# Optimization experiments

Measured on AMD Instinct MI355X. Metric: run time of the kernel, lower is better.

Reference implementation:

```python
import jax, jax.numpy as jnp
import numpy as np
from jax import lax

B, T, IN, H = 128, 1024, 130, 512


def setup_inputs() -> dict:
    key = jax.random.key(0)
    ks = jax.random.split(key, 6)
    inputs = jax.random.normal(ks[0], (B, T, IN), dtype=jnp.float32)
    # valid lengths in [1, T] (forward indexes outputs[len-1])
    inputs_len = jax.random.randint(ks[1], (B,), 1, T + 1)
    h0 = jnp.zeros((B, H), dtype=jnp.float32)
    c0 = jnp.zeros((B, H), dtype=jnp.float32)
    s = 1.0 / np.sqrt(H)
    W_ih = jax.random.uniform(ks[2], (4 * H, IN - 2), jnp.float32, -s, s)
    W_hh = jax.random.uniform(ks[3], (4 * H, H), jnp.float32, -s, s)
    b_ih = jax.random.uniform(ks[4], (4 * H,), jnp.float32, -s, s)
    b_hh = jax.random.uniform(ks[5], (4 * H,), jnp.float32, -s, s)
    return {"inputs": inputs, "inputs_len": inputs_len, "h0": h0, "c0": c0,
            "W_ih": W_ih, "W_hh": W_hh, "b_ih": b_ih, "b_hh": b_hh}


def _lstm_encode(inputs, h0, c0, W_ih, W_hh, b_ih, b_hh):
    # drop last 2 features (coordinates), as in stard_LSTM branch
    x = inputs[..., :-2]                                   # [B, T, IN-2]
    # precompute input projections for all timesteps (same math as per-step)
    xproj = jnp.einsum('bti,gi->tbg', x, W_ih) + b_ih + b_hh  # [T, B, 4H]

    def step(carry, xw):
        h, c = carry
        gates = xw + h @ W_hh.T                            # [B, 4H]
        i, f, g, o = jnp.split(gates, 4, axis=-1)
        i = jax.nn.sigmoid(i)
        f = jax.nn.sigmoid(f)
        g = jnp.tanh(g)
        o = jax.nn.sigmoid(o)
        c2 = f * c + i * g
        h2 = o * jnp.tanh(c2)
        return (h2, c2), h2

    _, hs = lax.scan(step, (h0, c0), xproj)                # hs: [T, B, H]
    return hs


def reference(inputs, inputs_len, h0, c0, W_ih, W_hh, b_ih, b_hh):
    hs = _lstm_encode(inputs, h0, c0, W_ih, W_hh, b_ih, b_hh)
    # gather hidden state at last valid timestep per sequence
    b_idx = jnp.arange(inputs.shape[0])
    return hs[inputs_len - 1, b_idx]                       # [B, H]
```

## Files before the change

### kernel.cpp

```cpp
#include <hip/hip_runtime.h>
#include <hip/hip_bf16.h>
#include <cstdint>
#include <cstddef>

#define T_STEPS 1024
#define BATCH   128
#define INF     128
#define HID     512
#define NBLK    256
#define NTHR    256
#define PK      648

typedef _Float16 f16x8 __attribute__((ext_vector_type(8)));
typedef float    f32x4 __attribute__((ext_vector_type(4)));

static __device__ __forceinline__ unsigned short f16b(float v) {
  _Float16 h = (_Float16)v;
  unsigned short u;
  __builtin_memcpy(&u, &h, 2);
  return u;
}
static __device__ __forceinline__ float fsigmoid(float x) {
  return 1.f / (1.f + __expf(-x));
}
static __device__ __forceinline__ float ftanh(float x) {
  return 1.f - 2.f / (__expf(2.f * x) + 1.f);
}


__global__ __launch_bounds__(256) void k_prep_x(const float* __restrict__ in,
                                                unsigned short* __restrict__ xp)
{
  int t = blockIdx.x >> 3, bg = blockIdx.x & 7;
  int tid = threadIdx.x;
  size_t base = (size_t)blockIdx.x * 2048;
  #pragma unroll
  for (int rep = 0; rep < 8; ++rep) {
    int idx = rep * 256 + tid;
    int c = idx >> 7, k = idx & 127;
    float v = in[((size_t)(bg * 16 + c) * T_STEPS + t) * 130 + k];
    xp[base + c * 128 + k] = f16b(v);
  }
}

__global__ __launch_bounds__(64) void k_prep_w(const float* __restrict__ Wih,
                                               const float* __restrict__ Whh,
                                               unsigned short* __restrict__ wf)
{
  int blk = blockIdx.x;
  int s = blk % 20; int r = blk / 20;
  int u4 = r & 3; int ug = r >> 2;
  int l = threadIdx.x;
  int m = l & 15;
  int Grow = (m & 3) * HID + ug * 16 + u4 * 4 + (m >> 2);
  int kb = s * 32 + (l >> 4) * 8;
  unsigned short o[8];
  #pragma unroll
  for (int j = 0; j < 8; ++j) {
    float v = (kb + j < INF) ? Wih[(size_t)Grow * INF + kb + j]
                             : Whh[(size_t)Grow * HID + (kb + j - INF)];
    o[j] = f16b(v);
  }
  unsigned short* d = wf + ((size_t)blk * 64 + l) * 8;
  #pragma unroll
  for (int j = 0; j < 8; ++j) d[j] = o[j];
}

__global__ __launch_bounds__(256) void k_prep_h(const float* __restrict__ h0,
                                                unsigned short* __restrict__ hp0,
                                                unsigned* __restrict__ flags)
{
  int idx = blockIdx.x * 256 + threadIdx.x;
  int bg = idx >> 13;
  int r = idx & 8191;
  int c = r >> 9, u = r & 511;
  hp0[idx] = f16b(h0[(size_t)(bg * 16 + c) * HID + u]);
  if (blockIdx.x == 0 && threadIdx.x < 256) flags[threadIdx.x] = 0;
}

__global__ __launch_bounds__(NTHR, 1) void k_persist(
    const unsigned short* __restrict__ xp,
    const unsigned short* __restrict__ wf,
    const float* __restrict__ bih, const float* __restrict__ bhh,
    unsigned short* __restrict__ hp0,
    unsigned short* __restrict__ hp1,
    const float* __restrict__ c0,
    const int* __restrict__ len,
    float* __restrict__ out,
    unsigned* __restrict__ flags)
{
  __shared__ short zpl[16][PK];

  const int blk = blockIdx.x;
  const int ug = blk & 31, bg = blk >> 5;
  const int tid = threadIdx.x;
  const int w = tid >> 6, l = tid & 63;
  const int cB = l & 15, gch = l >> 4;

  const uint4* wfq = (const uint4*)wf;
  const int fb = (ug * 4 + w) * 20;
#define LDW(s_) (*reinterpret_cast<const f16x8*>(&wfq[(size_t)(fb + (s_)) * 64 + l]))
  f16x8 A0 = LDW(0),  A1 = LDW(1),  A2 = LDW(2),  A3 = LDW(3),  A4 = LDW(4);
  f16x8 A5 = LDW(5),  A6 = LDW(6),  A7 = LDW(7),  A8 = LDW(8),  A9 = LDW(9);
  f16x8 A10 = LDW(10), A11 = LDW(11), A12 = LDW(12), A13 = LDW(13), A14 = LDW(14);
  f16x8 A15 = LDW(15), A16 = LDW(16), A17 = LDW(17), A18 = LDW(18), A19 = LDW(19);
#undef LDW
  asm volatile("" : "+v"(A0), "+v"(A1), "+v"(A2), "+v"(A3), "+v"(A4),
                    "+v"(A5), "+v"(A6), "+v"(A7), "+v"(A8), "+v"(A9),
                    "+v"(A10), "+v"(A11), "+v"(A12), "+v"(A13), "+v"(A14),
                    "+v"(A15), "+v"(A16), "+v"(A17), "+v"(A18), "+v"(A19));

  const int cb = l & 15;
  const int hu = ug * 16 + w * 4 + (l >> 4);
  const int gb = bg * 16 + cb;
  float c_reg = c0[(size_t)gb * HID + hu];
  const int mylen = len[gb];
  float bsq[4];
  #pragma unroll
  for (int g = 0; g < 4; ++g) bsq[g] = bih[g * HID + hu] + bhh[g * HID + hu];

  const unsigned* fl = flags + bg * 32;
  const int hc = tid >> 4, hj = tid & 15;

  for (int t = 0; t < T_STEPS; ++t) {
    uint4 xv = ((const uint4*)(xp + (size_t)(t * 8 + bg) * 2048))[tid];

    if (t) {
      const unsigned* fp = fl + (l & 31);
      for (;;) {
        unsigned v = __hip_atomic_load(fp, __ATOMIC_RELAXED,
                                       __HIP_MEMORY_SCOPE_AGENT);
        if (__all((int)(v >= (unsigned)t))) break;
        __builtin_amdgcn_s_sleep(1);
      }
    }
    const unsigned long long* hq =
        (const unsigned long long*)(((t & 1) ? hp1 : hp0) + (size_t)bg * 8192);
    unsigned* hdw = (unsigned*)(((t & 1) ? hp0 : hp1) + (size_t)bg * 8192);

    unsigned long long hch[8];
    #pragma unroll
    for (int k = 0; k < 8; ++k)
      hch[k] = __hip_atomic_load(hq + hc * 128 + hj * 8 + k,
                                 __ATOMIC_RELAXED, __HIP_MEMORY_SCOPE_AGENT);

    *(uint4*)((char*)&zpl[tid >> 4][0] + (tid & 15) * 16) = xv;
    #pragma unroll
    for (int k = 0; k < 8; ++k)
      *(unsigned long long*)(&zpl[hc][0] + 128 + hj * 32 + 4 * k) = hch[k];
    __syncthreads();

    f32x4 aE = {0, 0, 0, 0}, aO = {0, 0, 0, 0};
    const short* zr = &zpl[cB][0];
#define KS(s_, AF, ACC) \
  { f16x8 B = *(const f16x8*)(zr + (s_) * 32 + gch * 8); \
    ACC = __builtin_amdgcn_mfma_f32_16x16x32_f16(AF, B, ACC, 0, 0, 0); }
    KS(0, A0, aE)  KS(1, A1, aO)  KS(2, A2, aE)  KS(3, A3, aO)
    KS(4, A4, aE)  KS(5, A5, aO)  KS(6, A6, aE)  KS(7, A7, aO)
    KS(8, A8, aE)  KS(9, A9, aO)  KS(10, A10, aE) KS(11, A11, aO)
    KS(12, A12, aE) KS(13, A13, aO) KS(14, A14, aE) KS(15, A15, aO)
    KS(16, A16, aE) KS(17, A17, aO) KS(18, A18, aE) KS(19, A19, aO)
#undef KS

    float s0 = aE[0] + aO[0] + bsq[0];
    float s1 = aE[1] + aO[1] + bsq[1];
    float s2 = aE[2] + aO[2] + bsq[2];
    float s3 = aE[3] + aO[3] + bsq[3];
    float iv = fsigmoid(s0);
    float fv = fsigmoid(s1);
    float gv = ftanh(s2);
    float ov = fsigmoid(s3);
    c_reg = fv * c_reg + iv * gv;
    float h2 = ov * ftanh(c_reg);

    unsigned hb = f16b(h2);
    unsigned other = __shfl_xor(hb, 16);
    if (((l >> 4) & 1) == 0)
      __hip_atomic_store(hdw + cb * 256 + (hu >> 1), hb | (other << 16),
                         __ATOMIC_RELAXED, __HIP_MEMORY_SCOPE_AGENT);
    if (t == mylen - 1) out[(size_t)gb * HID + hu] = h2;

    __syncthreads();
    if (tid == 0)
      __hip_atomic_store((unsigned*)(flags + bg * 32 + ug), (unsigned)(t + 1),
                         __ATOMIC_RELAXED, __HIP_MEMORY_SCOPE_AGENT);
  }
}

extern "C" void kernel_launch(void* const* d_in, const int* in_sizes, int n_in,
                              void* d_out, int out_size, void* d_ws, size_t ws_size,
                              hipStream_t stream)
{
  const float* inputs = (const float*)d_in[0];
  const int*   len    = (const int*)  d_in[1];
  const float* h0     = (const float*)d_in[2];
  const float* c0     = (const float*)d_in[3];
  const float* Wih    = (const float*)d_in[4];
  const float* Whh    = (const float*)d_in[5];
  const float* bih    = (const float*)d_in[6];
  const float* bhh    = (const float*)d_in[7];
  float* out = (float*)d_out;

  char* p = (char*)d_ws;
  unsigned short* xp = (unsigned short*)p; p += (size_t)T_STEPS * 8 * 2048 * 2;
  unsigned short* wf = (unsigned short*)p; p += (size_t)2560 * 64 * 8 * 2;
  unsigned short* hp0 = (unsigned short*)p; p += (size_t)8 * 8192 * 2;
  unsigned short* hp1 = (unsigned short*)p; p += (size_t)8 * 8192 * 2;
  unsigned* flags = (unsigned*)p; p += 256 * 4;

  k_prep_x<<<T_STEPS * 8, 256, 0, stream>>>(inputs, xp);
  k_prep_w<<<2560, 64, 0, stream>>>(Wih, Whh, wf);
  k_prep_h<<<256, 256, 0, stream>>>(h0, hp0, flags);

  void* args[] = {(void*)&xp, (void*)&wf, (void*)&bih, (void*)&bhh,
                  (void*)&hp0, (void*)&hp1, (void*)&c0, (void*)&len,
                  (void*)&out, (void*)&flags};
  (void)hipLaunchCooperativeKernel((void*)k_persist, dim3(NBLK), dim3(NTHR),
                                   args, 0, stream);
}
```

Before: 3.270 ms.

## Replace per-block flag barrier with step-tagged hidden-state words

Each hidden-state pair is now stored as a 64-bit word that carries the step number in its upper half, so consumers poll the data words directly instead of waiting on per-block flags. This removes the trailing __syncthreads, the flag store and the separate flag spin from every step. The shared staging buffer is double-buffered so the next step's writes do not race readers of the previous step. In exchange the hidden-state traffic doubles in bytes, and correctness relies on the tagged 64-bit stores and loads being atomic.

```diff
diff --git a/kernel.cpp b/kernel.cpp
--- a/kernel.cpp
+++ b/kernel.cpp
@@ -67,29 +67,30 @@
 }
 
 __global__ __launch_bounds__(256) void k_prep_h(const float* __restrict__ h0,
-                                                unsigned short* __restrict__ hp0,
-                                                unsigned* __restrict__ flags)
+                                                unsigned long long* __restrict__ hp0,
+                                                unsigned long long* __restrict__ hp1)
 {
   int idx = blockIdx.x * 256 + threadIdx.x;
-  int bg = idx >> 13;
-  int r = idx & 8191;
-  int c = r >> 9, u = r & 511;
-  hp0[idx] = f16b(h0[(size_t)(bg * 16 + c) * HID + u]);
-  if (blockIdx.x == 0 && threadIdx.x < 256) flags[threadIdx.x] = 0;
+  int bg = idx >> 12;
+  int r = idx & 4095;
+  int c = r >> 8, u2 = r & 255;
+  float v0 = h0[(size_t)(bg * 16 + c) * HID + 2 * u2];
+  float v1 = h0[(size_t)(bg * 16 + c) * HID + 2 * u2 + 1];
+  hp0[idx] = (unsigned long long)((unsigned)f16b(v0) | ((unsigned)f16b(v1) << 16));
+  hp1[idx] = 0ull;
 }
 
 __global__ __launch_bounds__(NTHR, 1) void k_persist(
     const unsigned short* __restrict__ xp,
     const unsigned short* __restrict__ wf,
     const float* __restrict__ bih, const float* __restrict__ bhh,
-    unsigned short* __restrict__ hp0,
-    unsigned short* __restrict__ hp1,
+    unsigned long long* __restrict__ hp0,
+    unsigned long long* __restrict__ hp1,
     const float* __restrict__ c0,
     const int* __restrict__ len,
-    float* __restrict__ out,
-    unsigned* __restrict__ flags)
-{
-  __shared__ short zpl[16][PK];
+    float* __restrict__ out)
+{
+  __shared__ short zpl[2][16][PK];
 
   const int blk = blockIdx.x;
   const int ug = blk & 31, bg = blk >> 5;
@@ -111,7 +112,8 @@
                     "+v"(A15), "+v"(A16), "+v"(A17), "+v"(A18), "+v"(A19));
 
   const int cb = l & 15;
-  const int hu = ug * 16 + w * 4 + (l >> 4);
+  const int uloc = l >> 4;
+  const int hu = ug * 16 + w * 4 + uloc;
   const int gb = bg * 16 + cb;
   float c_reg = c0[(size_t)gb * HID + hu];
   const int mylen = len[gb];
@@ -119,39 +121,47 @@
   #pragma unroll
   for (int g = 0; g < 4; ++g) bsq[g] = bih[g * HID + hu] + bhh[g * HID + hu];
 
-  const unsigned* fl = flags + bg * 32;
-  const int hc = tid >> 4, hj = tid & 15;
+  const int hc = tid >> 4, hs = tid & 15;
 
   for (int t = 0; t < T_STEPS; ++t) {
+    const unsigned long long* hq = ((t & 1) ? hp1 : hp0) + (size_t)bg * 4096;
+    unsigned long long*       hd = ((t & 1) ? hp0 : hp1) + (size_t)bg * 4096;
+    short (*zb)[PK] = zpl[t & 1];
+
     uint4 xv = ((const uint4*)(xp + (size_t)(t * 8 + bg) * 2048))[tid];
 
-    if (t) {
-      const unsigned* fp = fl + (l & 31);
-      for (;;) {
-        unsigned v = __hip_atomic_load(fp, __ATOMIC_RELAXED,
-                                       __HIP_MEMORY_SCOPE_AGENT);
-        if (__all((int)(v >= (unsigned)t))) break;
-        __builtin_amdgcn_s_sleep(1);
-      }
+    unsigned long long hch[16];
+    #pragma unroll
+    for (int j = 0; j < 16; ++j)
+      hch[j] = __hip_atomic_load(hq + hc * 256 + j * 16 + hs,
+                                 __ATOMIC_RELAXED, __HIP_MEMORY_SCOPE_AGENT);
+
+    *(uint4*)((char*)&zb[tid >> 4][0] + (tid & 15) * 16) = xv;
+
+    for (;;) {
+      int bad = 0;
+      #pragma unroll
+      for (int j = 0; j < 16; ++j)
+        if ((unsigned)(hch[j] >> 32) != (unsigned)t) bad = 1;
+      if (!__any(bad)) break;
+      __builtin_amdgcn_s_sleep(1);
+      #pragma unroll
+      for (int j = 0; j < 16; ++j)
+        if ((unsigned)(hch[j] >> 32) != (unsigned)t)
+          hch[j] = __hip_atomic_load(hq + hc * 256 + j * 16 + hs,
+                                     __ATOMIC_RELAXED, __HIP_MEMORY_SCOPE_AGENT);
     }
-    const unsigned long long* hq =
-        (const unsigned long long*)(((t & 1) ? hp1 : hp0) + (size_t)bg * 8192);
-    unsigned* hdw = (unsigned*)(((t & 1) ? hp0 : hp1) + (size_t)bg * 8192);
-
-    unsigned long long hch[8];
-    #pragma unroll
-    for (int k = 0; k < 8; ++k)
-      hch[k] = __hip_atomic_load(hq + hc * 128 + hj * 8 + k,
-                                 __ATOMIC_RELAXED, __HIP_MEMORY_SCOPE_AGENT);
-
-    *(uint4*)((char*)&zpl[tid >> 4][0] + (tid & 15) * 16) = xv;
-    #pragma unroll
-    for (int k = 0; k < 8; ++k)
-      *(unsigned long long*)(&zpl[hc][0] + 128 + hj * 32 + 4 * k) = hch[k];
+
+    {
+      unsigned* zr = (unsigned*)&zb[hc][128];
+      #pragma unroll
+      for (int j = 0; j < 16; ++j)
+        zr[j * 16 + hs] = (unsigned)hch[j];
+    }
     __syncthreads();
 
     f32x4 aE = {0, 0, 0, 0}, aO = {0, 0, 0, 0};
-    const short* zr = &zpl[cB][0];
+    const short* zr = &zb[cB][0];
 #define KS(s_, AF, ACC) \
   { f16x8 B = *(const f16x8*)(zr + (s_) * 32 + gch * 8); \
     ACC = __builtin_amdgcn_mfma_f32_16x16x32_f16(AF, B, ACC, 0, 0, 0); }
@@ -175,15 +185,13 @@
 
     unsigned hb = f16b(h2);
     unsigned other = __shfl_xor(hb, 16);
-    if (((l >> 4) & 1) == 0)
-      __hip_atomic_store(hdw + cb * 256 + (hu >> 1), hb | (other << 16),
+    if ((uloc & 1) == 0) {
+      unsigned long long word = ((unsigned long long)(unsigned)(t + 1) << 32)
+                              | (unsigned long long)(hb | (other << 16));
+      __hip_atomic_store(hd + cb * 256 + (ug * 8 + w * 2 + (uloc >> 1)), word,
                          __ATOMIC_RELAXED, __HIP_MEMORY_SCOPE_AGENT);
+    }
     if (t == mylen - 1) out[(size_t)gb * HID + hu] = h2;
-
-    __syncthreads();
-    if (tid == 0)
-      __hip_atomic_store((unsigned*)(flags + bg * 32 + ug), (unsigned)(t + 1),
-                         __ATOMIC_RELAXED, __HIP_MEMORY_SCOPE_AGENT);
   }
 }
 
@@ -204,17 +212,16 @@
   char* p = (char*)d_ws;
   unsigned short* xp = (unsigned short*)p; p += (size_t)T_STEPS * 8 * 2048 * 2;
   unsigned short* wf = (unsigned short*)p; p += (size_t)2560 * 64 * 8 * 2;
-  unsigned short* hp0 = (unsigned short*)p; p += (size_t)8 * 8192 * 2;
-  unsigned short* hp1 = (unsigned short*)p; p += (size_t)8 * 8192 * 2;
-  unsigned* flags = (unsigned*)p; p += 256 * 4;
+  unsigned long long* hp0 = (unsigned long long*)p; p += (size_t)8 * 4096 * 8;
+  unsigned long long* hp1 = (unsigned long long*)p; p += (size_t)8 * 4096 * 8;
 
   k_prep_x<<<T_STEPS * 8, 256, 0, stream>>>(inputs, xp);
   k_prep_w<<<2560, 64, 0, stream>>>(Wih, Whh, wf);
-  k_prep_h<<<256, 256, 0, stream>>>(h0, hp0, flags);
+  k_prep_h<<<128, 256, 0, stream>>>(h0, hp0, hp1);
 
   void* args[] = {(void*)&xp, (void*)&wf, (void*)&bih, (void*)&bhh,
                   (void*)&hp0, (void*)&hp1, (void*)&c0, (void*)&len,
-                  (void*)&out, (void*)&flags};
+                  (void*)&out};
   (void)hipLaunchCooperativeKernel((void*)k_persist, dim3(NBLK), dim3(NTHR),
                                    args, 0, stream);
 }
```

New measurement: 3.452 ms. 5.6% more time.

## Split persistent LSTM across 512 blocks of two waves each

Applied to the files above, without the earlier changes.

Repartitions the persistent recurrent kernel from 256 blocks of 4 waves (16 hidden units each) to 512 blocks of 2 waves (8 hidden units each), using all CUs on the larger GPU. Weight prep layout, flag array, hidden-state staging loads and h writeback indexing are adjusted to match. The aim is to halve per-block MFMA work per step, at the cost of twice as many blocks to synchronise and each block staging more of the shared h vector per thread.

```diff
diff --git a/kernel.cpp b/kernel.cpp
--- a/kernel.cpp
+++ b/kernel.cpp
@@ -7,8 +7,8 @@
 #define BATCH   128
 #define INF     128
 #define HID     512
-#define NBLK    256
-#define NTHR    256
+#define NBLK    512
+#define NTHR    128
 #define PK      648
 
 typedef _Float16 f16x8 __attribute__((ext_vector_type(8)));
@@ -49,10 +49,10 @@
 {
   int blk = blockIdx.x;
   int s = blk % 20; int r = blk / 20;
-  int u4 = r & 3; int ug = r >> 2;
+  int w = r & 1; int ug = r >> 1;
   int l = threadIdx.x;
   int m = l & 15;
-  int Grow = (m & 3) * HID + ug * 16 + u4 * 4 + (m >> 2);
+  int Grow = (m & 3) * HID + ug * 8 + w * 4 + (m >> 2);
   int kb = s * 32 + (l >> 4) * 8;
   unsigned short o[8];
   #pragma unroll
@@ -75,7 +75,7 @@
   int r = idx & 8191;
   int c = r >> 9, u = r & 511;
   hp0[idx] = f16b(h0[(size_t)(bg * 16 + c) * HID + u]);
-  if (blockIdx.x == 0 && threadIdx.x < 256) flags[threadIdx.x] = 0;
+  if (idx < 512) flags[idx] = 0;
 }
 
 __global__ __launch_bounds__(NTHR, 1) void k_persist(
@@ -92,13 +92,13 @@
   __shared__ short zpl[16][PK];
 
   const int blk = blockIdx.x;
-  const int ug = blk & 31, bg = blk >> 5;
+  const int bg = blk >> 6, ug = blk & 63;
   const int tid = threadIdx.x;
   const int w = tid >> 6, l = tid & 63;
   const int cB = l & 15, gch = l >> 4;
 
   const uint4* wfq = (const uint4*)wf;
-  const int fb = (ug * 4 + w) * 20;
+  const int fb = (ug * 2 + w) * 20;
 #define LDW(s_) (*reinterpret_cast<const f16x8*>(&wfq[(size_t)(fb + (s_)) * 64 + l]))
   f16x8 A0 = LDW(0),  A1 = LDW(1),  A2 = LDW(2),  A3 = LDW(3),  A4 = LDW(4);
   f16x8 A5 = LDW(5),  A6 = LDW(6),  A7 = LDW(7),  A8 = LDW(8),  A9 = LDW(9);
@@ -111,7 +111,8 @@
                     "+v"(A15), "+v"(A16), "+v"(A17), "+v"(A18), "+v"(A19));
 
   const int cb = l & 15;
-  const int hu = ug * 16 + w * 4 + (l >> 4);
+  const int uloc = l >> 4;
+  const int hu = ug * 8 + w * 4 + uloc;
   const int gb = bg * 16 + cb;
   float c_reg = c0[(size_t)gb * HID + hu];
   const int mylen = len[gb];
@@ -119,14 +120,15 @@
   #pragma unroll
   for (int g = 0; g < 4; ++g) bsq[g] = bih[g * HID + hu] + bhh[g * HID + hu];
 
-  const unsigned* fl = flags + bg * 32;
-  const int hc = tid >> 4, hj = tid & 15;
+  const unsigned* fl = flags + bg * 64;
+  const int hc = tid >> 3, hs = tid & 7;
 
   for (int t = 0; t < T_STEPS; ++t) {
-    uint4 xv = ((const uint4*)(xp + (size_t)(t * 8 + bg) * 2048))[tid];
+    const uint4* xps = (const uint4*)(xp + (size_t)(t * 8 + bg) * 2048);
+    uint4 xa = xps[2 * tid], xb = xps[2 * tid + 1];
 
     if (t) {
-      const unsigned* fp = fl + (l & 31);
+      const unsigned* fp = fl + l;
       for (;;) {
         unsigned v = __hip_atomic_load(fp, __ATOMIC_RELAXED,
                                        __HIP_MEMORY_SCOPE_AGENT);
@@ -138,16 +140,20 @@
         (const unsigned long long*)(((t & 1) ? hp1 : hp0) + (size_t)bg * 8192);
     unsigned* hdw = (unsigned*)(((t & 1) ? hp0 : hp1) + (size_t)bg * 8192);
 
-    unsigned long long hch[8];
+    unsigned long long hch[16];
     #pragma unroll
-    for (int k = 0; k < 8; ++k)
-      hch[k] = __hip_atomic_load(hq + hc * 128 + hj * 8 + k,
+    for (int j = 0; j < 16; ++j)
+      hch[j] = __hip_atomic_load(hq + hc * 128 + j * 8 + hs,
                                  __ATOMIC_RELAXED, __HIP_MEMORY_SCOPE_AGENT);
 
-    *(uint4*)((char*)&zpl[tid >> 4][0] + (tid & 15) * 16) = xv;
+    {
+      int c_ = tid >> 3, k0 = (tid & 7) * 16;
+      *(uint4*)(&zpl[c_][k0])     = xa;
+      *(uint4*)(&zpl[c_][k0 + 8]) = xb;
+    }
     #pragma unroll
-    for (int k = 0; k < 8; ++k)
-      *(unsigned long long*)(&zpl[hc][0] + 128 + hj * 32 + 4 * k) = hch[k];
+    for (int j = 0; j < 16; ++j)
+      *(unsigned long long*)(&zpl[hc][128 + 4 * (j * 8 + hs)]) = hch[j];
     __syncthreads();
 
     f32x4 aE = {0, 0, 0, 0}, aO = {0, 0, 0, 0};
@@ -175,14 +181,15 @@
 
     unsigned hb = f16b(h2);
     unsigned other = __shfl_xor(hb, 16);
-    if (((l >> 4) & 1) == 0)
-      __hip_atomic_store(hdw + cb * 256 + (hu >> 1), hb | (other << 16),
+    if ((uloc & 1) == 0)
+      __hip_atomic_store(hdw + cb * 256 + (ug * 4 + w * 2 + (uloc >> 1)),
+                         hb | (other << 16),
                          __ATOMIC_RELAXED, __HIP_MEMORY_SCOPE_AGENT);
     if (t == mylen - 1) out[(size_t)gb * HID + hu] = h2;
 
     __syncthreads();
     if (tid == 0)
-      __hip_atomic_store((unsigned*)(flags + bg * 32 + ug), (unsigned)(t + 1),
+      __hip_atomic_store((unsigned*)(flags + bg * 64 + ug), (unsigned)(t + 1),
                          __ATOMIC_RELAXED, __HIP_MEMORY_SCOPE_AGENT);
   }
 }
@@ -206,7 +213,7 @@
   unsigned short* wf = (unsigned short*)p; p += (size_t)2560 * 64 * 8 * 2;
   unsigned short* hp0 = (unsigned short*)p; p += (size_t)8 * 8192 * 2;
   unsigned short* hp1 = (unsigned short*)p; p += (size_t)8 * 8192 * 2;
-  unsigned* flags = (unsigned*)p; p += 256 * 4;
+  unsigned* flags = (unsigned*)p; p += 512 * 4;
 
   k_prep_x<<<T_STEPS * 8, 256, 0, stream>>>(inputs, xp);
   k_prep_w<<<2560, 64, 0, stream>>>(Wih, Whh, wf);
```

Result: slower. 5.847 ms (+78.8%).
